# Optimization experiments

Measured on AMD Instinct MI355X. Metric: run time of the kernel, lower is better.

The kernel has to match this reference:

```python
import jax, jax.numpy as jnp
import numpy as np

NOISE_MULTIPLIER = 1.1
L2_NORM_CLIP = 1.0


def setup_inputs() -> dict:
    key = jax.random.key(0)
    inputs = jax.random.normal(key, (16384, 1024), dtype=jnp.float32)
    return {"inputs": inputs}


def reference(inputs) -> jnp.ndarray:
    B = inputs.shape[0]
    embed_flat = inputs.reshape(B, -1)  # [B, D]
    # per-sample L2 norm; scale = 1 / max(norm / clip, 1)
    norm = jnp.linalg.norm(embed_flat, ord=2, axis=-1)  # [B]
    scale = 1.0 / jnp.maximum(norm / L2_NORM_CLIP, 1.0)  # [B]
    # row-wise scaling == diag(scale) @ embed_flat, without the O(B^2) matmul
    clipped = (embed_flat * scale[:, None]).reshape(inputs.shape)
    noise_key = jax.random.key(42)
    noise = NOISE_MULTIPLIER * L2_NORM_CLIP * jax.random.normal(
        noise_key, inputs.shape, dtype=inputs.dtype
    )
    return clipped + noise
```

## Files before the change

### kernel.cpp

```cpp
#include <hip/hip_runtime.h>
#include <cstdint>
#include <cstddef>

#define ROWS 16384
#define COLS 1024

__device__ __forceinline__ uint32_t rotl32(uint32_t x, int r) {
    return __builtin_amdgcn_alignbit(x, x, 32 - r);
}

__device__ __forceinline__ void tf_round(uint32_t& x0, uint32_t& x1, int r) {
    x0 += x1;
    x1 = rotl32(x1, r);
    x1 ^= x0;
}

__device__ __forceinline__ uint32_t threefry_bits(uint32_t i) {
    const uint32_t ks1 = 42u;
    const uint32_t ks2 = 0x1BD11BF0u;

    uint32_t x1 = i + 42u;
    uint32_t x0 = x1;
    x1 = rotl32(x1, 13) ^ x0;
    tf_round(x0, x1, 15); tf_round(x0, x1, 26); tf_round(x0, x1, 6);
    x0 += ks1; x1 += ks2 + 1u;
    tf_round(x0, x1, 17); tf_round(x0, x1, 29); tf_round(x0, x1, 16); tf_round(x0, x1, 24);
    x0 += ks2; x1 += 2u;
    tf_round(x0, x1, 13); tf_round(x0, x1, 15); tf_round(x0, x1, 26); tf_round(x0, x1, 6);
     x1 += ks1 + 3u;
    tf_round(x0, x1, 17); tf_round(x0, x1, 29); tf_round(x0, x1, 16); tf_round(x0, x1, 24);
    x0 += ks1; x1 += ks2 + 4u;
    tf_round(x0, x1, 13); tf_round(x0, x1, 15); tf_round(x0, x1, 26); tf_round(x0, x1, 6);
    x0 += ks2; x1 += 5u;
    return x0 ^ x1;
}

__device__ __forceinline__ float ssq4(float4 a) {
    return fmaf(a.x, a.x, fmaf(a.y, a.y, fmaf(a.z, a.z, a.w * a.w)));
}

struct ErfC {
    float k0,k1,k2,k3,k4,k5,k6,k7,k8, ln2;
};

__device__ __forceinline__ ErfC make_coefs() {
    ErfC c;
    c.k0 = 4.3716863e-08f;
    c.k1 = 5.3400890e-07f;
    c.k2 = -5.4811046e-06f;
    c.k3 = -6.8315807e-06f;
    c.k4 = 3.4003203e-04f;
    c.k5 = -1.9503385e-03f;
    c.k6 = -6.4989473e-03f;
    c.k7 = 3.8368293e-01f;
    c.k8 = 2.3356449e+00f;
    c.ln2 = 0.69314718f;
    asm("" : "+s"(c.k0), "+s"(c.k1), "+s"(c.k2), "+s"(c.k3), "+s"(c.k4),
             "+s"(c.k5), "+s"(c.k6), "+s"(c.k7), "+s"(c.k8), "+s"(c.ln2));
    return c;
}

__device__ __forceinline__ float bits_to_noise(uint32_t bits, const ErfC& c) {
    uint32_t fb = (bits >> 9) | 0x3f800000u;
    float u = __uint_as_float(fb) - 1.0f;
    const float minval = -0.99999994f;
    float v = fmaf(u, 2.0f, minval);
    float t = fmaf(-v, v, 1.0f);
    float w = -c.ln2 * __log2f(t);

    float z = w - 2.5f;
    float p = c.k0;
    p = fmaf(p, z, c.k1);
    p = fmaf(p, z, c.k2);
    p = fmaf(p, z, c.k3);
    p = fmaf(p, z, c.k4);
    p = fmaf(p, z, c.k5);
    p = fmaf(p, z, c.k6);
    p = fmaf(p, z, c.k7);
    p = fmaf(p, z, c.k8);

    if (w >= 5.0f) {
        float s = __builtin_amdgcn_sqrtf(w) - 3.0f;
        float q = -3.1146030e-04f;
        q = fmaf(q, s, 1.5704224e-04f);
        q = fmaf(q, s, 2.0990855e-03f);
        q = fmaf(q, s, -5.7144932e-03f);
        q = fmaf(q, s, 8.9285939e-03f);
        q = fmaf(q, s, -1.1857797e-02f);
        q = fmaf(q, s, 1.4683435e-02f);
        q = fmaf(q, s, 1.5582439e+00f);
        q = fmaf(q, s, 4.4070777e+00f);
        p = q;
    }
    return p * v;
}

__device__ __forceinline__ float4 noise4(uint32_t idx0, const ErfC& c) {
    float4 n;
    n.x = bits_to_noise(threefry_bits(idx0 + 0u), c);
    n.y = bits_to_noise(threefry_bits(idx0 + 1u), c);
    n.z = bits_to_noise(threefry_bits(idx0 + 2u), c);
    n.w = bits_to_noise(threefry_bits(idx0 + 3u), c);
    return n;
}

__global__ void __launch_bounds__(256)
gaussian_dp_kernel(const float* __restrict__ in, float* __restrict__ out) {
    const int wid  = threadIdx.x >> 6;
    const int lane = threadIdx.x & 63;
    const int r    = (blockIdx.x << 2) + wid;

    const float4* inR = reinterpret_cast<const float4*>(in + (size_t)r * COLS);
    float4 a0 = inR[lane];
    float4 a1 = inR[lane + 64];
    float4 a2 = inR[lane + 128];
    float4 a3 = inR[lane + 192];

    float ssq = (ssq4(a0) + ssq4(a1)) + (ssq4(a2) + ssq4(a3));

    #pragma unroll
    for (int off = 32; off > 0; off >>= 1) {
        ssq += __shfl_xor(ssq, off, 64);
    }

    const float scale = 1.0f / fmaxf(sqrtf(ssq), 1.0f);

    const ErfC c = make_coefs();

    const uint32_t base = ((uint32_t)r << 10) + ((uint32_t)lane << 2);

    float4* outR = reinterpret_cast<float4*>(out + (size_t)r * COLS);

    {
        float4 n = noise4(base, c);
        float4 o;
        o.x = fmaf(a0.x, scale, n.x); o.y = fmaf(a0.y, scale, n.y);
        o.z = fmaf(a0.z, scale, n.z); o.w = fmaf(a0.w, scale, n.w);
        outR[lane] = o;
    }
    {
        float4 n = noise4(base + 256u, c);
        float4 o;
        o.x = fmaf(a1.x, scale, n.x); o.y = fmaf(a1.y, scale, n.y);
        o.z = fmaf(a1.z, scale, n.z); o.w = fmaf(a1.w, scale, n.w);
        outR[lane + 64] = o;
    }
    {
        float4 n = noise4(base + 512u, c);
        float4 o;
        o.x = fmaf(a2.x, scale, n.x); o.y = fmaf(a2.y, scale, n.y);
        o.z = fmaf(a2.z, scale, n.z); o.w = fmaf(a2.w, scale, n.w);
        outR[lane + 128] = o;
    }
    {
        float4 n = noise4(base + 768u, c);
        float4 o;
        o.x = fmaf(a3.x, scale, n.x); o.y = fmaf(a3.y, scale, n.y);
        o.z = fmaf(a3.z, scale, n.z); o.w = fmaf(a3.w, scale, n.w);
        outR[lane + 192] = o;
    }
}

extern "C" void kernel_launch(void* const* d_in, const int* in_sizes, int n_in,
                              void* d_out, int out_size, void* d_ws, size_t ws_size,
                              hipStream_t stream) {
    const float* in = (const float*)d_in[0];
    float* out = (float*)d_out;
    gaussian_dp_kernel<<<ROWS / 4, 256, 0, stream>>>(in, out);
}
```

Measured before the change: 42.61 us.

## Shorten inverse-erf polynomial and compute noise before norm reduction

Replaces the degree-8 inverse-erf central polynomial with a degree-4 fit in the log2 domain, which folds away the ln2 multiply and the z shift. It uses an int-to-float conversion for the uniform and moves noise generation ahead of the row-norm reduction, so the ALU work can overlap the shuffle chain and the loads. The lower-degree approximation may reduce accuracy of the Gaussian samples versus the reference, and holding all 16 noise values live raises register pressure.

```diff
diff --git a/kernel.cpp b/kernel.cpp
--- a/kernel.cpp
+++ b/kernel.cpp
@@ -35,51 +35,20 @@
     return x0 ^ x1;
 }
 
-__device__ __forceinline__ float ssq4(float4 a) {
-    return fmaf(a.x, a.x, fmaf(a.y, a.y, fmaf(a.z, a.z, a.w * a.w)));
-}
+__device__ __forceinline__ float bits_to_noise(uint32_t bits) {
+    float fm = (float)(bits >> 9);
+    float v  = fmaf(fm, 2.3841858e-07f, -0.99999994f);
+    float t  = fmaf(-v, v, 1.0f);
+    float y  = __log2f(t) + 3.6067376f;
 
-struct ErfC {
-    float k0,k1,k2,k3,k4,k5,k6,k7,k8, ln2;
-};
+    float p;
+    p = fmaf(7.84913e-05f, y, 6.49511e-04f);
+    p = fmaf(p, y, -3.12243e-03f);
+    p = fmaf(p, y, -2.6594862e-01f);
+    p = fmaf(p, y, 2.3356449e+00f);
 
-__device__ __forceinline__ ErfC make_coefs() {
-    ErfC c;
-    c.k0 = 4.3716863e-08f;
-    c.k1 = 5.3400890e-07f;
-    c.k2 = -5.4811046e-06f;
-    c.k3 = -6.8315807e-06f;
-    c.k4 = 3.4003203e-04f;
-    c.k5 = -1.9503385e-03f;
-    c.k6 = -6.4989473e-03f;
-    c.k7 = 3.8368293e-01f;
-    c.k8 = 2.3356449e+00f;
-    c.ln2 = 0.69314718f;
-    asm("" : "+s"(c.k0), "+s"(c.k1), "+s"(c.k2), "+s"(c.k3), "+s"(c.k4),
-             "+s"(c.k5), "+s"(c.k6), "+s"(c.k7), "+s"(c.k8), "+s"(c.ln2));
-    return c;
-}
-
-__device__ __forceinline__ float bits_to_noise(uint32_t bits, const ErfC& c) {
-    uint32_t fb = (bits >> 9) | 0x3f800000u;
-    float u = __uint_as_float(fb) - 1.0f;
-    const float minval = -0.99999994f;
-    float v = fmaf(u, 2.0f, minval);
-    float t = fmaf(-v, v, 1.0f);
-    float w = -c.ln2 * __log2f(t);
-
-    float z = w - 2.5f;
-    float p = c.k0;
-    p = fmaf(p, z, c.k1);
-    p = fmaf(p, z, c.k2);
-    p = fmaf(p, z, c.k3);
-    p = fmaf(p, z, c.k4);
-    p = fmaf(p, z, c.k5);
-    p = fmaf(p, z, c.k6);
-    p = fmaf(p, z, c.k7);
-    p = fmaf(p, z, c.k8);
-
-    if (w >= 5.0f) {
+    if (y <= -3.6067376f) {
+        float w = fmaf(-0.69314718f, y, 2.5f);
         float s = __builtin_amdgcn_sqrtf(w) - 3.0f;
         float q = -3.1146030e-04f;
         q = fmaf(q, s, 1.5704224e-04f);
@@ -95,13 +64,17 @@
     return p * v;
 }
 
-__device__ __forceinline__ float4 noise4(uint32_t idx0, const ErfC& c) {
+__device__ __forceinline__ float4 noise4(uint32_t idx0) {
     float4 n;
-    n.x = bits_to_noise(threefry_bits(idx0 + 0u), c);
-    n.y = bits_to_noise(threefry_bits(idx0 + 1u), c);
-    n.z = bits_to_noise(threefry_bits(idx0 + 2u), c);
-    n.w = bits_to_noise(threefry_bits(idx0 + 3u), c);
+    n.x = bits_to_noise(threefry_bits(idx0 + 0u));
+    n.y = bits_to_noise(threefry_bits(idx0 + 1u));
+    n.z = bits_to_noise(threefry_bits(idx0 + 2u));
+    n.w = bits_to_noise(threefry_bits(idx0 + 3u));
     return n;
+}
+
+__device__ __forceinline__ float ssq4(float4 a) {
+    return fmaf(a.x, a.x, fmaf(a.y, a.y, fmaf(a.z, a.z, a.w * a.w)));
 }
 
 __global__ void __launch_bounds__(256)
@@ -116,6 +89,13 @@
     float4 a2 = inR[lane + 128];
     float4 a3 = inR[lane + 192];
 
+    const uint32_t base = ((uint32_t)r << 10) + ((uint32_t)lane << 2);
+
+    float4 n0 = noise4(base);
+    float4 n1 = noise4(base + 256u);
+    float4 n2 = noise4(base + 512u);
+    float4 n3 = noise4(base + 768u);
+
     float ssq = (ssq4(a0) + ssq4(a1)) + (ssq4(a2) + ssq4(a3));
 
     #pragma unroll
@@ -123,42 +103,26 @@
         ssq += __shfl_xor(ssq, off, 64);
     }
 
-    const float scale = 1.0f / fmaxf(sqrtf(ssq), 1.0f);
-
-    const ErfC c = make_coefs();
-
-    const uint32_t base = ((uint32_t)r << 10) + ((uint32_t)lane << 2);
+    const float scale = 1.0f / fmaxf(__builtin_amdgcn_sqrtf(ssq), 1.0f);
 
     float4* outR = reinterpret_cast<float4*>(out + (size_t)r * COLS);
 
-    {
-        float4 n = noise4(base, c);
-        float4 o;
-        o.x = fmaf(a0.x, scale, n.x); o.y = fmaf(a0.y, scale, n.y);
-        o.z = fmaf(a0.z, scale, n.z); o.w = fmaf(a0.w, scale, n.w);
-        outR[lane] = o;
-    }
-    {
-        float4 n = noise4(base + 256u, c);
-        float4 o;
-        o.x = fmaf(a1.x, scale, n.x); o.y = fmaf(a1.y, scale, n.y);
-        o.z = fmaf(a1.z, scale, n.z); o.w = fmaf(a1.w, scale, n.w);
-        outR[lane + 64] = o;
-    }
-    {
-        float4 n = noise4(base + 512u, c);
-        float4 o;
-        o.x = fmaf(a2.x, scale, n.x); o.y = fmaf(a2.y, scale, n.y);
-        o.z = fmaf(a2.z, scale, n.z); o.w = fmaf(a2.w, scale, n.w);
-        outR[lane + 128] = o;
-    }
-    {
-        float4 n = noise4(base + 768u, c);
-        float4 o;
-        o.x = fmaf(a3.x, scale, n.x); o.y = fmaf(a3.y, scale, n.y);
-        o.z = fmaf(a3.z, scale, n.z); o.w = fmaf(a3.w, scale, n.w);
-        outR[lane + 192] = o;
-    }
+    float4 o;
+    o.x = fmaf(a0.x, scale, n0.x); o.y = fmaf(a0.y, scale, n0.y);
+    o.z = fmaf(a0.z, scale, n0.z); o.w = fmaf(a0.w, scale, n0.w);
+    outR[lane] = o;
+
+    o.x = fmaf(a1.x, scale, n1.x); o.y = fmaf(a1.y, scale, n1.y);
+    o.z = fmaf(a1.z, scale, n1.z); o.w = fmaf(a1.w, scale, n1.w);
+    outR[lane + 64] = o;
+
+    o.x = fmaf(a2.x, scale, n2.x); o.y = fmaf(a2.y, scale, n2.y);
+    o.z = fmaf(a2.z, scale, n2.z); o.w = fmaf(a2.w, scale, n2.w);
+    outR[lane + 128] = o;
+
+    o.x = fmaf(a3.x, scale, n3.x); o.y = fmaf(a3.y, scale, n3.y);
+    o.z = fmaf(a3.z, scale, n3.z); o.w = fmaf(a3.w, scale, n3.w);
+    outR[lane + 192] = o;
 }
 
 extern "C" void kernel_launch(void* const* d_in, const int* in_sizes, int n_in,
```

New measurement: 41.00 us. 1.04x faster.
